# Kernel optimization log

Hardware: AMD Instinct MI355X
Metric: run time of the kernel (lower is better)

The kernel has to match this reference:

```python
import jax, jax.numpy as jnp
import numpy as np

B, N, D, H, E, K = 8, 4096, 128, 256, 16, 2


def setup_inputs() -> dict:
    key = jax.random.key(0)
    ks = jax.random.split(key, 11)
    sc = 0.05
    return {
        "x":   jax.random.normal(ks[0], (B, N, D), jnp.float32),
        "Wg":  jax.random.normal(ks[1], (D, E), jnp.float32) * sc,
        "bg":  jnp.zeros((E,), jnp.float32),
        "W1":  jax.random.normal(ks[2], (E, D, H), jnp.float32) * sc,
        "b1":  jnp.zeros((E, H), jnp.float32),
        "W2":  jax.random.normal(ks[3], (E, H, D), jnp.float32) * sc,
        "b2":  jnp.zeros((E, D), jnp.float32),
        "Wu1": jax.random.normal(ks[4], (D, H), jnp.float32) * sc,
        "bu1": jnp.zeros((H,), jnp.float32),
        "Wu2": jax.random.normal(ks[5], (H, D), jnp.float32) * sc,
        "bu2": jnp.zeros((D,), jnp.float32),
    }


def reference(x, Wg, bg, W1, b1, W2, b2, Wu1, bu1, Wu2, bu2):
    b, n, d = x.shape
    xt = x.reshape(b * n, d)                       # [T, D]
    T = xt.shape[0]

    # gating: top-k logits kept, rest -inf, then softmax -> zeros off top-k
    logits = xt @ Wg + bg                          # [T, E]
    topv, topi = jax.lax.top_k(logits, K)          # [T, K]
    mask = jnp.full_like(logits, -jnp.inf)
    mask = mask.at[jnp.arange(T)[:, None], topi].set(topv)
    gate = jax.nn.softmax(mask, axis=-1)           # [T, E]

    # dense all-expert MLP (matches original torch.stack over experts)
    h = jax.nn.relu(jnp.einsum('td,edh->teh', xt, W1) + b1)   # [T, E, H]
    eo = jnp.einsum('teh,ehd->ted', h, W2) + b2               # [T, E, D]

    # universal expert scaled by omega = 1 - max gate
    omega = 1.0 - jnp.max(gate, axis=1, keepdims=True)        # [T, 1]
    uni = omega * (jax.nn.relu(xt @ Wu1 + bu1) @ Wu2 + bu2)   # [T, D]

    out = jnp.einsum('te,ted->td', gate, eo) + uni
    return out.reshape(b, n, d)
```

## Files before the change

kernel.cpp:

```cpp
#include <hip/hip_runtime.h>
#include <hip/hip_bf16.h>

constexpr int kT = 32768;
constexpr int kD = 128;
constexpr int kH = 256;
constexpr int kE = 16;

typedef __bf16 bf16x8 __attribute__((ext_vector_type(8)));
typedef unsigned short u16x8 __attribute__((ext_vector_type(8)));
typedef unsigned short u16x4 __attribute__((ext_vector_type(4)));
typedef float f32x4 __attribute__((ext_vector_type(4)));

#define LDX 136
#define LDQ 72

constexpr int NB_TP   = 272;
constexpr int NB_GATE = kT / 64;
constexpr int CNT_STRIDE = 32;
constexpr int EXP_GRID = 1040;

__device__ __forceinline__ unsigned short f2bf(float f) {
  unsigned int u = __float_as_uint(f);
  u += 0x7FFFu + ((u >> 16) & 1u);
  return (unsigned short)(u >> 16);
}
__device__ __forceinline__ float bf2f(unsigned short s) {
  return __uint_as_float((unsigned int)s << 16);
}
__device__ __forceinline__ void bar_lgkm() {
  asm volatile("s_waitcnt lgkmcnt(0)" ::: "memory");
  __builtin_amdgcn_s_barrier();
  asm volatile("" ::: "memory");
}

__global__ __launch_bounds__(256) void front_kernel(
    const float* __restrict__ x, const float* __restrict__ Wg,
    const float* __restrict__ bg,
    const float* __restrict__ W1, const float* __restrict__ W2,
    const float* __restrict__ Wu1, const float* __restrict__ Wu2,
    unsigned short* __restrict__ xb, unsigned short* __restrict__ W1t,
    unsigned short* __restrict__ W2t, unsigned short* __restrict__ Wu1t,
    unsigned short* __restrict__ Wu2t,
    int* __restrict__ cnt, int* __restrict__ btok, float* __restrict__ bgate,
    int* __restrict__ tpos, float* __restrict__ omega)
{
  __shared__ __align__(16) char smem[46848];
  const int tid = threadIdx.x;
  const int b = blockIdx.x;

  if (b < NB_TP) {
    int bb = b;
    const float* src; unsigned short* dst; int R, C, r0, c0;
    if (bb < 136) {
      int m = bb >> 3, t8 = bb & 7;
      R = 128; C = 256;
      src = (m < 16) ? W1 + (size_t)m * 32768 : Wu1;
      dst = (m < 16) ? W1t + (size_t)m * 32768 : Wu1t;
      r0 = (t8 & 1) * 64; c0 = (t8 >> 1) * 64;
    } else {
      bb -= 136;
      int m = bb >> 3, t8 = bb & 7;
      R = 256; C = 128;
      src = (m < 16) ? W2 + (size_t)m * 32768 : Wu2;
      dst = (m < 16) ? W2t + (size_t)m * 32768 : Wu2t;
      r0 = (t8 >> 1) * 64; c0 = (t8 & 1) * 64;
    }
    unsigned short (*tl)[72] = reinterpret_cast<unsigned short(*)[72]>(smem);
#pragma unroll
    for (int i = 0; i < 4; ++i) {
      int s = i * 256 + tid;
      int r = s >> 4, c4 = s & 15;
      float4 v = *reinterpret_cast<const float4*>(&src[(size_t)(r0 + r) * C + c0 + c4 * 4]);
      tl[c4 * 4 + 0][r] = f2bf(v.x);
      tl[c4 * 4 + 1][r] = f2bf(v.y);
      tl[c4 * 4 + 2][r] = f2bf(v.z);
      tl[c4 * 4 + 3][r] = f2bf(v.w);
    }
    __syncthreads();
#pragma unroll
    for (int i = 0; i < 2; ++i) {
      int s = i * 256 + tid;
      int c = s >> 3, seg = s & 7;
      uint4 v = *reinterpret_cast<const uint4*>(&tl[c][seg * 8]);
      *reinterpret_cast<uint4*>(&dst[(size_t)(c0 + c) * R + r0 + seg * 8]) = v;
    }
    return;
  }

  {
    float* sWt = reinterpret_cast<float*>(smem);
    float* sX  = reinterpret_cast<float*>(smem + 8448);
    float* sL  = reinterpret_cast<float*>(smem + 42240);
    int* hcnt  = reinterpret_cast<int*>(smem + 46592);
    int* hbase = reinterpret_cast<int*>(smem + 46656);
    const int t0 = (b - NB_TP) * 64;

    if (tid < kE) hcnt[tid] = 0;
    for (int i = tid; i < kD * kE; i += 256) {
      int d = i >> 4, e = i & 15;
      sWt[e * 132 + d] = Wg[i];
    }
    const float4* xv = reinterpret_cast<const float4*>(x + (size_t)t0 * kD);
    for (int i = tid; i < 64 * kD / 4; i += 256) {
      int r = i >> 5, c4 = i & 31;
      *reinterpret_cast<float4*>(&sX[r * 132 + c4 * 4]) = xv[i];
    }
    __syncthreads();

    const int e = tid & 15, tq = tid >> 4;
    const double bgd = (double)bg[e];
    const float4* wr = reinterpret_cast<const float4*>(&sWt[e * 132]);
    double acc[4] = {0.0, 0.0, 0.0, 0.0};
#pragma unroll
    for (int d4 = 0; d4 < 32; ++d4) {
      float4 wa = wr[d4];
#pragma unroll
      for (int p = 0; p < 4; ++p) {
        float4 xa = *reinterpret_cast<const float4*>(&sX[(p * 16 + tq) * 132 + d4 * 4]);
        acc[p] += (double)xa.x * (double)wa.x + (double)xa.y * (double)wa.y
                + (double)xa.z * (double)wa.z + (double)xa.w * (double)wa.w;
      }
    }
#pragma unroll
    for (int p = 0; p < 4; ++p)
      sL[(p * 16 + tq) * 17 + e] = (float)(acc[p] + bgd);
#pragma unroll
    for (int p = 0; p < 4; ++p) {
      int idx = p * 256 + tid;
      int r = idx >> 4, c8 = (idx & 15) * 8;
      const float* sp = &sX[r * 132 + c8];
      u16x8 v;
#pragma unroll
      for (int j = 0; j < 8; ++j) v[j] = f2bf(sp[j]);
      *reinterpret_cast<u16x8*>(&xb[(size_t)(t0 + r) * kD + c8]) = v;
    }
    __syncthreads();

    int e0 = 0, e1 = 0, lp0 = 0, lp1 = 0;
    float g0 = 0.f, g1 = 0.f;
    const int t = t0 + tid;
    if (tid < 64) {
      float v0 = -3.4e38f, v1 = -3.4e38f;
      for (int i = 0; i < kE; ++i) {
        float v = sL[tid * 17 + i];
        if (v > v0) { v1 = v0; e1 = e0; v0 = v; e0 = i; }
        else if (v > v1) { v1 = v; e1 = i; }
      }
      float r = expf(v1 - v0);
      g0 = 1.f / (1.f + r);
      g1 = 1.f - g0;
      omega[t] = 1.f - g0;
      lp0 = atomicAdd(&hcnt[e0], 1);
      lp1 = atomicAdd(&hcnt[e1], 1);
    }
    __syncthreads();
    if (tid < kE)
      hbase[tid] = atomicAdd(&cnt[tid * CNT_STRIDE], hcnt[tid]);
    __syncthreads();
    if (tid < 64) {
      int p0 = hbase[e0] + lp0;
      btok[e0 * kT + p0] = t; bgate[e0 * kT + p0] = g0;
      int p1 = hbase[e1] + lp1;
      btok[e1 * kT + p1] = t; bgate[e1 * kT + p1] = g1;
      tpos[2 * t]     = (e0 << 16) | p0;
      tpos[2 * t + 1] = (e1 << 16) | p1;
    }
  }
}

#define LOAD_W1(BUF, HQ)                                                      \
  _Pragma("unroll")                                                           \
  for (int kk = 0; kk < 4; ++kk)                                              \
    W1r[BUF][kk] = *reinterpret_cast<const bf16x8*>(                          \
        Bw1 + (size_t)((HQ) * 64 + w * 16 + lr) * kD + kk * 32 + lg * 8);

#define LOAD_W2(BUF, HQ)                                                      \
  _Pragma("unroll")                                                           \
  for (int n = 0; n < 2; ++n)                                                 \
    _Pragma("unroll")                                                         \
    for (int k2 = 0; k2 < 2; ++k2)                                            \
      W2r[BUF][n * 2 + k2] = *reinterpret_cast<const bf16x8*>(                \
          Bw2 + (size_t)(w * 32 + n * 16 + lr) * kH + (HQ) * 64 + k2 * 32 + lg * 8);

__global__ __launch_bounds__(256) void moe_expert_kernel(
    const unsigned short* __restrict__ xb,
    const unsigned short* __restrict__ W1t,
    const unsigned short* __restrict__ W2t,
    const float* __restrict__ b1, const float* __restrict__ b2,
    const int* __restrict__ cnt, const int* __restrict__ btok,
    const float* __restrict__ bgate,
    unsigned short* __restrict__ eo)
{
  __shared__ alignas(16) char smem[27136];
  unsigned short* xs = reinterpret_cast<unsigned short*>(smem);
  unsigned short* hs = reinterpret_cast<unsigned short*>(smem + 17408);
  int*   toks = reinterpret_cast<int*>(smem + 26624);
  float* gts  = reinterpret_cast<float*>(smem + 26880);
  unsigned short* stB = reinterpret_cast<unsigned short*>(smem);
  const int tid = threadIdx.x;
  const int bid = blockIdx.x;

  int c16[16];
#pragma unroll
  for (int i = 0; i < 16; ++i) c16[i] = cnt[i * CNT_STRIDE];
  int e = -1, tile = 0, eobase = 0, accb = 0;
#pragma unroll
  for (int i = 0; i < 16; ++i) {
    int tl = (c16[i] + 63) >> 6;
    if (e < 0) {
      if (bid < accb + tl) { e = i; tile = bid - accb; }
      else { accb += tl; eobase += c16[i]; }
    }
  }
  if (e < 0) return;
  const int rows = min(64, c16[e] - tile * 64);

  const int w = tid >> 6, l = tid & 63, lr = l & 15, lg = l >> 4;
  const int gr = tid >> 4, gc = (tid & 15) * 8;
  const f32x4 z4 = {0.f, 0.f, 0.f, 0.f};

  const unsigned short* Bw1 = W1t + (size_t)e * kH * kD;
  const unsigned short* Bw2 = W2t + (size_t)e * kD * kH;
  const float* bs1 = b1 + (size_t)e * kH;
  const float* bs2 = b2 + (size_t)e * kD;

  bf16x8 W1r[2][4], W2r[2][4];
  LOAD_W1(0, 0); LOAD_W2(0, 0);
  float b1q[4];
#pragma unroll
  for (int hq = 0; hq < 4; ++hq) b1q[hq] = bs1[hq * 64 + w * 16 + lr];
  float b2v[2];
#pragma unroll
  for (int n = 0; n < 2; ++n) b2v[n] = bs2[w * 32 + n * 16 + lr];

  {
    int tokR[4]; float gtR[4];
#pragma unroll
    for (int p = 0; p < 4; ++p) {
      int r = p * 16 + gr; bool v = r < rows; int bi2 = e * kT + tile * 64 + r;
      tokR[p] = v ? btok[bi2] : 0;
      gtR[p]  = v ? bgate[bi2] : 0.f;
    }
#pragma unroll
    for (int p = 0; p < 4; ++p) {
      uint4 v = *reinterpret_cast<const uint4*>(xb + (size_t)tokR[p] * kD + gc);
      *reinterpret_cast<uint4*>(&xs[(p * 16 + gr) * LDX + gc]) = v;
    }
    if ((tid & 15) == 0) {
#pragma unroll
      for (int p = 0; p < 4; ++p) {
        toks[p * 16 + gr] = tokR[p];
        gts[p * 16 + gr]  = gtR[p];
      }
    }
  }
  f32x4 acc2[4][2];
#pragma unroll
  for (int m = 0; m < 4; ++m)
#pragma unroll
    for (int n = 0; n < 2; ++n) acc2[m][n] = z4;
  bar_lgkm();

#pragma unroll
  for (int hq = 0; hq < 4; ++hq) {
    const int cur = hq & 1;
    if (hq < 3) {
      const int nxt = cur ^ 1;
      LOAD_W1(nxt, hq + 1);
      LOAD_W2(nxt, hq + 1);
    }
    f32x4 acc[4];
#pragma unroll
    for (int m = 0; m < 4; ++m) acc[m] = z4;
#pragma unroll
    for (int kk = 0; kk < 4; ++kk) {
      bf16x8 a[4];
#pragma unroll
      for (int m = 0; m < 4; ++m)
        a[m] = *reinterpret_cast<const bf16x8*>(xs + (m * 16 + lr) * LDX + kk * 32 + lg * 8);
#pragma unroll
      for (int m = 0; m < 4; ++m)
        acc[m] = __builtin_amdgcn_mfma_f32_16x16x32_bf16(a[m], W1r[cur][kk], acc[m], 0, 0, 0);
    }
#pragma unroll
    for (int m = 0; m < 4; ++m)
#pragma unroll
      for (int q = 0; q < 4; ++q) {
        float v = acc[m][q] + b1q[hq];
        v = fmaxf(v, 0.f);
        hs[(m * 16 + lg * 4 + q) * LDQ + w * 16 + lr] = f2bf(v);
      }
    bar_lgkm();
#pragma unroll
    for (int k2 = 0; k2 < 2; ++k2) {
      bf16x8 a[4];
#pragma unroll
      for (int m = 0; m < 4; ++m)
        a[m] = *reinterpret_cast<const bf16x8*>(hs + (m * 16 + lr) * LDQ + k2 * 32 + lg * 8);
#pragma unroll
      for (int m = 0; m < 4; ++m)
#pragma unroll
        for (int n = 0; n < 2; ++n)
          acc2[m][n] = __builtin_amdgcn_mfma_f32_16x16x32_bf16(a[m], W2r[cur][n * 2 + k2], acc2[m][n], 0, 0, 0);
    }
    bar_lgkm();
  }

#pragma unroll
  for (int m = 0; m < 4; ++m)
#pragma unroll
    for (int q = 0; q < 4; ++q) {
      int r = m * 16 + lg * 4 + q;
      float g = gts[r];
#pragma unroll
      for (int n = 0; n < 2; ++n)
        stB[r * LDX + w * 32 + n * 16 + lr] = f2bf(g * (acc2[m][n][q] + b2v[n]));
    }
  bar_lgkm();
  unsigned short* dst = eo + (size_t)(eobase + tile * 64) * kD;
#pragma unroll
  for (int j = 0; j < 4; ++j) {
    int gidx = j * 256 + tid;
    int r = gidx >> 4, seg = gidx & 15;
    if (r < rows) {
      uint4 v = *reinterpret_cast<const uint4*>(&stB[r * LDX + seg * 8]);
      *reinterpret_cast<uint4*>(dst + (size_t)r * kD + seg * 8) = v;
    }
  }
}

__global__ __launch_bounds__(256) void uni_combine_kernel(
    const unsigned short* __restrict__ xb,
    const unsigned short* __restrict__ Wu1t,
    const unsigned short* __restrict__ Wu2t,
    const float* __restrict__ bu1, const float* __restrict__ bu2,
    const float* __restrict__ omega, const int* __restrict__ cnt,
    const int* __restrict__ tpos, const unsigned short* __restrict__ eo,
    float* __restrict__ out)
{
  __shared__ alignas(16) char smem[27456];
  unsigned short* xs = reinterpret_cast<unsigned short*>(smem);
  unsigned short* hs = reinterpret_cast<unsigned short*>(smem + 17408);
  float* sOm  = reinterpret_cast<float*>(smem + 26624);
  int*   sTp  = reinterpret_cast<int*>(smem + 26880);
  int*   sBase= reinterpret_cast<int*>(smem + 27392);
  float* stF  = reinterpret_cast<float*>(smem);
  const int tid = threadIdx.x;
  const int t0 = blockIdx.x * 64;

  const int w = tid >> 6, l = tid & 63, lr = l & 15, lg = l >> 4;
  const int gr = tid >> 4, gc = (tid & 15) * 8;
  const f32x4 z4 = {0.f, 0.f, 0.f, 0.f};

  const unsigned short* Bw1 = Wu1t;
  const unsigned short* Bw2 = Wu2t;
  bf16x8 W1r[2][4], W2r[2][4];
  LOAD_W1(0, 0); LOAD_W2(0, 0);
  float b1q[4];
#pragma unroll
  for (int hq = 0; hq < 4; ++hq) b1q[hq] = bu1[hq * 64 + w * 16 + lr];
  float b2v[2];
#pragma unroll
  for (int n = 0; n < 2; ++n) b2v[n] = bu2[w * 32 + n * 16 + lr];

  if (tid < 16) {
    int s = 0;
    for (int i = 0; i < tid; ++i) s += cnt[i * CNT_STRIDE];
    sBase[tid] = s;
  }
  if (tid >= 64 && tid < 128) sOm[tid - 64] = omega[t0 + tid - 64];
  if (tid >= 128) sTp[tid - 128] = tpos[2 * t0 + tid - 128];
#pragma unroll
  for (int p = 0; p < 4; ++p) {
    uint4 v = *reinterpret_cast<const uint4*>(xb + (size_t)(t0 + p * 16 + gr) * kD + gc);
    *reinterpret_cast<uint4*>(&xs[(p * 16 + gr) * LDX + gc]) = v;
  }
  f32x4 acc2[4][2];
#pragma unroll
  for (int m = 0; m < 4; ++m)
#pragma unroll
    for (int n = 0; n < 2; ++n) acc2[m][n] = z4;
  bar_lgkm();

#pragma unroll
  for (int hq = 0; hq < 4; ++hq) {
    const int cur = hq & 1;
    if (hq < 3) {
      const int nxt = cur ^ 1;
      LOAD_W1(nxt, hq + 1);
      LOAD_W2(nxt, hq + 1);
    }
    f32x4 acc[4];
#pragma unroll
    for (int m = 0; m < 4; ++m) acc[m] = z4;
#pragma unroll
    for (int kk = 0; kk < 4; ++kk) {
      bf16x8 a[4];
#pragma unroll
      for (int m = 0; m < 4; ++m)
        a[m] = *reinterpret_cast<const bf16x8*>(xs + (m * 16 + lr) * LDX + kk * 32 + lg * 8);
#pragma unroll
      for (int m = 0; m < 4; ++m)
        acc[m] = __builtin_amdgcn_mfma_f32_16x16x32_bf16(a[m], W1r[cur][kk], acc[m], 0, 0, 0);
    }
#pragma unroll
    for (int m = 0; m < 4; ++m)
#pragma unroll
      for (int q = 0; q < 4; ++q) {
        float v = acc[m][q] + b1q[hq];
        v = fmaxf(v, 0.f);
        hs[(m * 16 + lg * 4 + q) * LDQ + w * 16 + lr] = f2bf(v);
      }
    bar_lgkm();
#pragma unroll
    for (int k2 = 0; k2 < 2; ++k2) {
      bf16x8 a[4];
#pragma unroll
      for (int m = 0; m < 4; ++m)
        a[m] = *reinterpret_cast<const bf16x8*>(hs + (m * 16 + lr) * LDQ + k2 * 32 + lg * 8);
#pragma unroll
      for (int m = 0; m < 4; ++m)
#pragma unroll
        for (int n = 0; n < 2; ++n)
          acc2[m][n] = __builtin_amdgcn_mfma_f32_16x16x32_bf16(a[m], W2r[cur][n * 2 + k2], acc2[m][n], 0, 0, 0);
    }
    bar_lgkm();
  }

#pragma unroll
  for (int ch = 0; ch < 2; ++ch) {
    if ((w >> 1) == ch) {
#pragma unroll
      for (int m = 0; m < 4; ++m)
#pragma unroll
        for (int q = 0; q < 4; ++q) {
          int r = m * 16 + lg * 4 + q;
          float om = sOm[r];
#pragma unroll
          for (int n = 0; n < 2; ++n)
            stF[r * 68 + (w & 1) * 32 + n * 16 + lr] = om * (acc2[m][n][q] + b2v[n]);
        }
    }
    bar_lgkm();
#pragma unroll
    for (int j = 0; j < 4; ++j) {
      int gidx = j * 256 + tid;
      int r = gidx >> 4, seg = gidx & 15;
      int a0 = sTp[2 * r], a1 = sTp[2 * r + 1];
      size_t e0r = (size_t)(sBase[a0 >> 16] + (a0 & 0xffff)) * kD + ch * 64 + seg * 4;
      size_t e1r = (size_t)(sBase[a1 >> 16] + (a1 & 0xffff)) * kD + ch * 64 + seg * 4;
      u16x4 v0 = *reinterpret_cast<const u16x4*>(eo + e0r);
      u16x4 v1 = *reinterpret_cast<const u16x4*>(eo + e1r);
      float4 v = *reinterpret_cast<const float4*>(&stF[r * 68 + seg * 4]);
      v.x += bf2f(v0[0]) + bf2f(v1[0]);
      v.y += bf2f(v0[1]) + bf2f(v1[1]);
      v.z += bf2f(v0[2]) + bf2f(v1[2]);
      v.w += bf2f(v0[3]) + bf2f(v1[3]);
      *reinterpret_cast<float4*>(out + (size_t)(t0 + r) * kD + ch * 64 + seg * 4) = v;
    }
    bar_lgkm();
  }
}

extern "C" void kernel_launch(void* const* d_in, const int* in_sizes, int n_in,
                              void* d_out, int out_size, void* d_ws, size_t ws_size,
                              hipStream_t stream) {
  (void)in_sizes; (void)n_in; (void)out_size; (void)ws_size;
  const float* x   = (const float*)d_in[0];
  const float* Wg  = (const float*)d_in[1];
  const float* bg  = (const float*)d_in[2];
  const float* W1  = (const float*)d_in[3];
  const float* b1  = (const float*)d_in[4];
  const float* W2  = (const float*)d_in[5];
  const float* b2  = (const float*)d_in[6];
  const float* Wu1 = (const float*)d_in[7];
  const float* bu1 = (const float*)d_in[8];
  const float* Wu2 = (const float*)d_in[9];
  const float* bu2 = (const float*)d_in[10];
  float* out = (float*)d_out;

  char* ws = (char*)d_ws;
  constexpr size_t OFF_XB    = 0;
  constexpr size_t OFF_W1T   = 8388608;
  constexpr size_t OFF_W2T   = 9437184;
  constexpr size_t OFF_WU1T  = 10485760;
  constexpr size_t OFF_WU2T  = 10551296;
  constexpr size_t OFF_CNT   = 10616832;
  constexpr size_t OFF_TPOS  = 10620928;
  constexpr size_t OFF_BTOK  = 10883072;
  constexpr size_t OFF_BGATE = 13111296;
  constexpr size_t OFF_EO    = 15339520;
  constexpr size_t OFF_OM    = 32116736;

  unsigned short* xb   = (unsigned short*)(ws + OFF_XB);
  unsigned short* W1t  = (unsigned short*)(ws + OFF_W1T);
  unsigned short* W2t  = (unsigned short*)(ws + OFF_W2T);
  unsigned short* Wu1t = (unsigned short*)(ws + OFF_WU1T);
  unsigned short* Wu2t = (unsigned short*)(ws + OFF_WU2T);
  int*   cnt   = (int*)(ws + OFF_CNT);
  int*   tpos  = (int*)(ws + OFF_TPOS);
  int*   btok  = (int*)(ws + OFF_BTOK);
  float* bgate = (float*)(ws + OFF_BGATE);
  unsigned short* eo = (unsigned short*)(ws + OFF_EO);
  float* omega = (float*)(ws + OFF_OM);

  hipMemsetAsync(cnt, 0, kE * CNT_STRIDE * sizeof(int), stream);
  front_kernel<<<NB_TP + NB_GATE, 256, 0, stream>>>(
      x, Wg, bg, W1, W2, Wu1, Wu2,
      xb, W1t, W2t, Wu1t, Wu2t, cnt, btok, bgate, tpos, omega);
  moe_expert_kernel<<<EXP_GRID, 256, 0, stream>>>(
      xb, W1t, W2t, b1, b2, cnt, btok, bgate, eo);
  uni_combine_kernel<<<kT / 64, 256, 0, stream>>>(
      xb, Wu1t, Wu2t, bu1, bu2, omega, cnt, tpos, eo, out);
}
```

Baseline: 69.27 us.

## Repartition expert MLP so each wave owns 16 token rows, removing block barriers

The expert kernel previously split the hidden and output columns across the four waves, with every wave sharing all 64 token rows. That required a block-wide barrier around the shared hidden tile for each of four chunks. Now each wave owns 16 token rows and computes the full hidden and output width itself. The hidden activations go through a per-wave LDS slice, so no inter-wave barriers are needed in the main loop, and the MFMA operands are swapped so results come out transposed and vector-stored. In exchange, each wave now loads the full W1 and W2 fragments directly from global memory (4x more weight traffic per block, likely cached) without prefetch double-buffering, which raises register pressure and load latency exposure.

```diff
diff --git a/kernel.cpp b/kernel.cpp
--- a/kernel.cpp
+++ b/kernel.cpp
@@ -13,6 +13,7 @@
 
 #define LDX 136
 #define LDQ 72
+#define LDW 70
 
 constexpr int NB_TP   = 272;
 constexpr int NB_GATE = kT / 64;
@@ -168,20 +169,6 @@
   }
 }
 
-#define LOAD_W1(BUF, HQ)                                                      \
-  _Pragma("unroll")                                                           \
-  for (int kk = 0; kk < 4; ++kk)                                              \
-    W1r[BUF][kk] = *reinterpret_cast<const bf16x8*>(                          \
-        Bw1 + (size_t)((HQ) * 64 + w * 16 + lr) * kD + kk * 32 + lg * 8);
-
-#define LOAD_W2(BUF, HQ)                                                      \
-  _Pragma("unroll")                                                           \
-  for (int n = 0; n < 2; ++n)                                                 \
-    _Pragma("unroll")                                                         \
-    for (int k2 = 0; k2 < 2; ++k2)                                            \
-      W2r[BUF][n * 2 + k2] = *reinterpret_cast<const bf16x8*>(                \
-          Bw2 + (size_t)(w * 32 + n * 16 + lr) * kH + (HQ) * 64 + k2 * 32 + lg * 8);
-
 __global__ __launch_bounds__(256) void moe_expert_kernel(
     const unsigned short* __restrict__ xb,
     const unsigned short* __restrict__ W1t,
@@ -191,9 +178,9 @@
     const float* __restrict__ bgate,
     unsigned short* __restrict__ eo)
 {
-  __shared__ alignas(16) char smem[27136];
+  __shared__ alignas(16) char smem[27392];
   unsigned short* xs = reinterpret_cast<unsigned short*>(smem);
-  unsigned short* hs = reinterpret_cast<unsigned short*>(smem + 17408);
+  unsigned short* hsAll = reinterpret_cast<unsigned short*>(smem + 17408);
   int*   toks = reinterpret_cast<int*>(smem + 26624);
   float* gts  = reinterpret_cast<float*>(smem + 26880);
   unsigned short* stB = reinterpret_cast<unsigned short*>(smem);
@@ -218,21 +205,13 @@
   const int w = tid >> 6, l = tid & 63, lr = l & 15, lg = l >> 4;
   const int gr = tid >> 4, gc = (tid & 15) * 8;
   const f32x4 z4 = {0.f, 0.f, 0.f, 0.f};
+  unsigned short* hsw = hsAll + w * 16 * LDW;
 
   const unsigned short* Bw1 = W1t + (size_t)e * kH * kD;
   const unsigned short* Bw2 = W2t + (size_t)e * kD * kH;
   const float* bs1 = b1 + (size_t)e * kH;
   const float* bs2 = b2 + (size_t)e * kD;
 
-  bf16x8 W1r[2][4], W2r[2][4];
-  LOAD_W1(0, 0); LOAD_W2(0, 0);
-  float b1q[4];
-#pragma unroll
-  for (int hq = 0; hq < 4; ++hq) b1q[hq] = bs1[hq * 64 + w * 16 + lr];
-  float b2v[2];
-#pragma unroll
-  for (int n = 0; n < 2; ++n) b2v[n] = bs2[w * 32 + n * 16 + lr];
-
   {
     int tokR[4]; float gtR[4];
 #pragma unroll
@@ -254,68 +233,71 @@
       }
     }
   }
-  f32x4 acc2[4][2];
-#pragma unroll
-  for (int m = 0; m < 4; ++m)
-#pragma unroll
-    for (int n = 0; n < 2; ++n) acc2[m][n] = z4;
   bar_lgkm();
 
-#pragma unroll
-  for (int hq = 0; hq < 4; ++hq) {
-    const int cur = hq & 1;
-    if (hq < 3) {
-      const int nxt = cur ^ 1;
-      LOAD_W1(nxt, hq + 1);
-      LOAD_W2(nxt, hq + 1);
-    }
+  bf16x8 xr[4];
+#pragma unroll
+  for (int kk = 0; kk < 4; ++kk)
+    xr[kk] = *reinterpret_cast<const bf16x8*>(xs + (w * 16 + lr) * LDX + kk * 32 + lg * 8);
+  const float g = gts[w * 16 + lr];
+
+  f32x4 acc2[8];
+#pragma unroll
+  for (int n = 0; n < 8; ++n) acc2[n] = z4;
+
+#pragma unroll
+  for (int c = 0; c < 4; ++c) {
+    bf16x8 W1f[4][4];
+#pragma unroll
+    for (int n = 0; n < 4; ++n)
+#pragma unroll
+      for (int kk = 0; kk < 4; ++kk)
+        W1f[n][kk] = *reinterpret_cast<const bf16x8*>(
+            Bw1 + (size_t)(c * 64 + n * 16 + lr) * kD + kk * 32 + lg * 8);
     f32x4 acc[4];
 #pragma unroll
-    for (int m = 0; m < 4; ++m) acc[m] = z4;
-#pragma unroll
-    for (int kk = 0; kk < 4; ++kk) {
-      bf16x8 a[4];
-#pragma unroll
-      for (int m = 0; m < 4; ++m)
-        a[m] = *reinterpret_cast<const bf16x8*>(xs + (m * 16 + lr) * LDX + kk * 32 + lg * 8);
-#pragma unroll
-      for (int m = 0; m < 4; ++m)
-        acc[m] = __builtin_amdgcn_mfma_f32_16x16x32_bf16(a[m], W1r[cur][kk], acc[m], 0, 0, 0);
-    }
-#pragma unroll
-    for (int m = 0; m < 4; ++m)
-#pragma unroll
-      for (int q = 0; q < 4; ++q) {
-        float v = acc[m][q] + b1q[hq];
-        v = fmaxf(v, 0.f);
-        hs[(m * 16 + lg * 4 + q) * LDQ + w * 16 + lr] = f2bf(v);
-      }
-    bar_lgkm();
-#pragma unroll
-    for (int k2 = 0; k2 < 2; ++k2) {
-      bf16x8 a[4];
-#pragma unroll
-      for (int m = 0; m < 4; ++m)
-        a[m] = *reinterpret_cast<const bf16x8*>(hs + (m * 16 + lr) * LDQ + k2 * 32 + lg * 8);
-#pragma unroll
-      for (int m = 0; m < 4; ++m)
-#pragma unroll
-        for (int n = 0; n < 2; ++n)
-          acc2[m][n] = __builtin_amdgcn_mfma_f32_16x16x32_bf16(a[m], W2r[cur][n * 2 + k2], acc2[m][n], 0, 0, 0);
-    }
-    bar_lgkm();
-  }
-
-#pragma unroll
-  for (int m = 0; m < 4; ++m)
-#pragma unroll
-    for (int q = 0; q < 4; ++q) {
-      int r = m * 16 + lg * 4 + q;
-      float g = gts[r];
-#pragma unroll
-      for (int n = 0; n < 2; ++n)
-        stB[r * LDX + w * 32 + n * 16 + lr] = f2bf(g * (acc2[m][n][q] + b2v[n]));
-    }
+    for (int n = 0; n < 4; ++n) acc[n] = z4;
+#pragma unroll
+    for (int kk = 0; kk < 4; ++kk)
+#pragma unroll
+      for (int n = 0; n < 4; ++n)
+        acc[n] = __builtin_amdgcn_mfma_f32_16x16x32_bf16(W1f[n][kk], xr[kk], acc[n], 0, 0, 0);
+#pragma unroll
+    for (int n = 0; n < 4; ++n) {
+      f32x4 b1s = *reinterpret_cast<const f32x4*>(bs1 + c * 64 + n * 16 + lg * 4);
+      u16x4 hv;
+#pragma unroll
+      for (int q = 0; q < 4; ++q)
+        hv[q] = f2bf(fmaxf(acc[n][q] + b1s[q], 0.f));
+      *reinterpret_cast<u16x4*>(&hsw[lr * LDW + n * 16 + lg * 4]) = hv;
+    }
+    bf16x8 W2f[8][2];
+#pragma unroll
+    for (int n = 0; n < 8; ++n)
+#pragma unroll
+      for (int k2 = 0; k2 < 2; ++k2)
+        W2f[n][k2] = *reinterpret_cast<const bf16x8*>(
+            Bw2 + (size_t)(n * 16 + lr) * kH + c * 64 + k2 * 32 + lg * 8);
+    bf16x8 a2[2];
+#pragma unroll
+    for (int k2 = 0; k2 < 2; ++k2)
+      a2[k2] = *reinterpret_cast<const bf16x8*>(hsw + lr * LDW + k2 * 32 + lg * 8);
+#pragma unroll
+    for (int k2 = 0; k2 < 2; ++k2)
+#pragma unroll
+      for (int n = 0; n < 8; ++n)
+        acc2[n] = __builtin_amdgcn_mfma_f32_16x16x32_bf16(W2f[n][k2], a2[k2], acc2[n], 0, 0, 0);
+  }
+
+#pragma unroll
+  for (int n = 0; n < 8; ++n) {
+    f32x4 b2s = *reinterpret_cast<const f32x4*>(bs2 + n * 16 + lg * 4);
+    u16x4 sv;
+#pragma unroll
+    for (int q = 0; q < 4; ++q)
+      sv[q] = f2bf(g * (acc2[n][q] + b2s[q]));
+    *reinterpret_cast<u16x4*>(&stB[(w * 16 + lr) * LDX + n * 16 + lg * 4]) = sv;
+  }
   bar_lgkm();
   unsigned short* dst = eo + (size_t)(eobase + tile * 64) * kD;
 #pragma unroll
@@ -328,6 +310,20 @@
     }
   }
 }
+
+#define LOAD_W1U(BUF, HQ)                                                     \
+  _Pragma("unroll")                                                           \
+  for (int kk = 0; kk < 4; ++kk)                                              \
+    W1r[BUF][kk] = *reinterpret_cast<const bf16x8*>(                          \
+        Bw1 + (size_t)((HQ) * 64 + w * 16 + lr) * kD + kk * 32 + lg * 8);
+
+#define LOAD_W2U(BUF, HQ)                                                     \
+  _Pragma("unroll")                                                           \
+  for (int n = 0; n < 2; ++n)                                                 \
+    _Pragma("unroll")                                                         \
+    for (int k2 = 0; k2 < 2; ++k2)                                            \
+      W2r[BUF][n * 2 + k2] = *reinterpret_cast<const bf16x8*>(                \
+          Bw2 + (size_t)(w * 32 + n * 16 + lr) * kH + (HQ) * 64 + k2 * 32 + lg * 8);
 
 __global__ __launch_bounds__(256) void uni_combine_kernel(
     const unsigned short* __restrict__ xb,
@@ -355,7 +351,7 @@
   const unsigned short* Bw1 = Wu1t;
   const unsigned short* Bw2 = Wu2t;
   bf16x8 W1r[2][4], W2r[2][4];
-  LOAD_W1(0, 0); LOAD_W2(0, 0);
+  LOAD_W1U(0, 0); LOAD_W2U(0, 0);
   float b1q[4];
 #pragma unroll
   for (int hq = 0; hq < 4; ++hq) b1q[hq] = bu1[hq * 64 + w * 16 + lr];
@@ -387,8 +383,8 @@
     const int cur = hq & 1;
     if (hq < 3) {
       const int nxt = cur ^ 1;
-      LOAD_W1(nxt, hq + 1);
-      LOAD_W2(nxt, hq + 1);
+      LOAD_W1U(nxt, hq + 1);
+      LOAD_W2U(nxt, hq + 1);
     }
     f32x4 acc[4];
 #pragma unroll
```

After: 123.5 us. +78.2%, slower.

## Scatter bf16 token rows into per-expert gathered buffer during gating

Applied to the files above, without the earlier changes.

The gating kernel now writes each token's bf16 activation row directly into a per-expert contiguous slot buffer (xg), replacing the btok index list. The expert kernel then loads its tile rows contiguously instead of gathering through token indices, which removes a dependent index load and the random-access gather from the expert kernel's critical path. In exchange, the front kernel does extra scattered 16-byte writes (two copies per token) and needs a larger workspace. Rows past the valid count in a tile may read uninitialized xg data, but their gates are zero.

```diff
diff --git a/kernel.cpp b/kernel.cpp
--- a/kernel.cpp
+++ b/kernel.cpp
@@ -41,8 +41,9 @@
     unsigned short* __restrict__ xb, unsigned short* __restrict__ W1t,
     unsigned short* __restrict__ W2t, unsigned short* __restrict__ Wu1t,
     unsigned short* __restrict__ Wu2t,
-    int* __restrict__ cnt, int* __restrict__ btok, float* __restrict__ bgate,
-    int* __restrict__ tpos, float* __restrict__ omega)
+    int* __restrict__ cnt, float* __restrict__ bgate,
+    int* __restrict__ tpos, float* __restrict__ omega,
+    unsigned short* __restrict__ xg)
 {
   __shared__ __align__(16) char smem[46848];
   const int tid = threadIdx.x;
@@ -91,6 +92,7 @@
     float* sWt = reinterpret_cast<float*>(smem);
     float* sX  = reinterpret_cast<float*>(smem + 8448);
     float* sL  = reinterpret_cast<float*>(smem + 42240);
+    int* sSlot = reinterpret_cast<int*>(smem + 42240);
     int* hcnt  = reinterpret_cast<int*>(smem + 46592);
     int* hbase = reinterpret_cast<int*>(smem + 46656);
     const int t0 = (b - NB_TP) * 64;
@@ -159,11 +161,24 @@
     __syncthreads();
     if (tid < 64) {
       int p0 = hbase[e0] + lp0;
-      btok[e0 * kT + p0] = t; bgate[e0 * kT + p0] = g0;
+      bgate[e0 * kT + p0] = g0;
       int p1 = hbase[e1] + lp1;
-      btok[e1 * kT + p1] = t; bgate[e1 * kT + p1] = g1;
+      bgate[e1 * kT + p1] = g1;
       tpos[2 * t]     = (e0 << 16) | p0;
       tpos[2 * t + 1] = (e1 << 16) | p1;
+      sSlot[2 * tid]     = e0 * kT + p0;
+      sSlot[2 * tid + 1] = e1 * kT + p1;
+    }
+    __syncthreads();
+    for (int i = tid; i < 128 * 16; i += 256) {
+      int sl = i >> 4, seg = i & 15;
+      int r = sl >> 1;
+      int slot = sSlot[sl];
+      const float* sp = &sX[r * 132 + seg * 8];
+      u16x8 v;
+#pragma unroll
+      for (int j = 0; j < 8; ++j) v[j] = f2bf(sp[j]);
+      *reinterpret_cast<u16x8*>(xg + (size_t)slot * kD + seg * 8) = v;
     }
   }
 }
@@ -183,18 +198,16 @@
           Bw2 + (size_t)(w * 32 + n * 16 + lr) * kH + (HQ) * 64 + k2 * 32 + lg * 8);
 
 __global__ __launch_bounds__(256) void moe_expert_kernel(
-    const unsigned short* __restrict__ xb,
+    const unsigned short* __restrict__ xg,
     const unsigned short* __restrict__ W1t,
     const unsigned short* __restrict__ W2t,
     const float* __restrict__ b1, const float* __restrict__ b2,
-    const int* __restrict__ cnt, const int* __restrict__ btok,
-    const float* __restrict__ bgate,
+    const int* __restrict__ cnt, const float* __restrict__ bgate,
     unsigned short* __restrict__ eo)
 {
   __shared__ alignas(16) char smem[27136];
   unsigned short* xs = reinterpret_cast<unsigned short*>(smem);
   unsigned short* hs = reinterpret_cast<unsigned short*>(smem + 17408);
-  int*   toks = reinterpret_cast<int*>(smem + 26624);
   float* gts  = reinterpret_cast<float*>(smem + 26880);
   unsigned short* stB = reinterpret_cast<unsigned short*>(smem);
   const int tid = threadIdx.x;
@@ -234,24 +247,21 @@
   for (int n = 0; n < 2; ++n) b2v[n] = bs2[w * 32 + n * 16 + lr];
 
   {
-    int tokR[4]; float gtR[4];
+    float gtR[4];
 #pragma unroll
     for (int p = 0; p < 4; ++p) {
-      int r = p * 16 + gr; bool v = r < rows; int bi2 = e * kT + tile * 64 + r;
-      tokR[p] = v ? btok[bi2] : 0;
-      gtR[p]  = v ? bgate[bi2] : 0.f;
+      int r = p * 16 + gr;
+      gtR[p] = (r < rows) ? bgate[e * kT + tile * 64 + r] : 0.f;
     }
 #pragma unroll
     for (int p = 0; p < 4; ++p) {
-      uint4 v = *reinterpret_cast<const uint4*>(xb + (size_t)tokR[p] * kD + gc);
+      uint4 v = *reinterpret_cast<const uint4*>(
+          xg + (size_t)(e * kT + tile * 64 + p * 16 + gr) * kD + gc);
       *reinterpret_cast<uint4*>(&xs[(p * 16 + gr) * LDX + gc]) = v;
     }
     if ((tid & 15) == 0) {
 #pragma unroll
-      for (int p = 0; p < 4; ++p) {
-        toks[p * 16 + gr] = tokR[p];
-        gts[p * 16 + gr]  = gtR[p];
-      }
+      for (int p = 0; p < 4; ++p) gts[p * 16 + gr] = gtR[p];
     }
   }
   f32x4 acc2[4][2];
@@ -487,10 +497,10 @@
   constexpr size_t OFF_WU2T  = 10551296;
   constexpr size_t OFF_CNT   = 10616832;
   constexpr size_t OFF_TPOS  = 10620928;
-  constexpr size_t OFF_BTOK  = 10883072;
   constexpr size_t OFF_BGATE = 13111296;
   constexpr size_t OFF_EO    = 15339520;
   constexpr size_t OFF_OM    = 32116736;
+  constexpr size_t OFF_XG    = 33554432;
 
   unsigned short* xb   = (unsigned short*)(ws + OFF_XB);
   unsigned short* W1t  = (unsigned short*)(ws + OFF_W1T);
@@ -499,17 +509,17 @@
   unsigned short* Wu2t = (unsigned short*)(ws + OFF_WU2T);
   int*   cnt   = (int*)(ws + OFF_CNT);
   int*   tpos  = (int*)(ws + OFF_TPOS);
-  int*   btok  = (int*)(ws + OFF_BTOK);
   float* bgate = (float*)(ws + OFF_BGATE);
   unsigned short* eo = (unsigned short*)(ws + OFF_EO);
   float* omega = (float*)(ws + OFF_OM);
+  unsigned short* xg = (unsigned short*)(ws + OFF_XG);
 
   hipMemsetAsync(cnt, 0, kE * CNT_STRIDE * sizeof(int), stream);
   front_kernel<<<NB_TP + NB_GATE, 256, 0, stream>>>(
       x, Wg, bg, W1, W2, Wu1, Wu2,
-      xb, W1t, W2t, Wu1t, Wu2t, cnt, btok, bgate, tpos, omega);
+      xb, W1t, W2t, Wu1t, Wu2t, cnt, bgate, tpos, omega, xg);
   moe_expert_kernel<<<EXP_GRID, 256, 0, stream>>>(
-      xb, W1t, W2t, b1, b2, cnt, btok, bgate, eo);
+      xg, W1t, W2t, b1, b2, cnt, bgate, eo);
   uni_combine_kernel<<<kT / 64, 256, 0, stream>>>(
       xb, Wu1t, Wu2t, bu1, bu2, omega, cnt, tpos, eo, out);
 }
```

New measurement: 71.81 us. 3.7% more time.
